# Performance work log

Measured on AMD Instinct MI355X. Metric: run time of the kernel, lower is better.

## Reference

```python
import jax, jax.numpy as jnp
import numpy as np


def hsigmoid(x):
    # ReLU6(x + 3) / 6
    return jnp.clip(x + 3.0, 0.0, 6.0) / 6.0


def setup_inputs() -> dict:
    key = jax.random.key(0)
    k1, k2 = jax.random.split(key)
    B, C, H, W = 16, 256, 128, 128
    K = 7
    x = jax.random.normal(k1, (B, C, H, W), dtype=jnp.float32)
    # Kaiming-ish small init for the 2->1 7x7 conv
    conv_w = jax.random.normal(k2, (1, 2, K, K), dtype=jnp.float32) * (1.0 / np.sqrt(2 * K * K))
    conv_b = jnp.zeros((1,), dtype=jnp.float32)
    return {"x": x, "conv_w": conv_w, "conv_b": conv_b}


def reference(x, conv_w, conv_b):
    # channel-wise max and mean -> [B, 1, H, W] each
    max_x = jnp.max(x, axis=1, keepdims=True)
    avg_x = jnp.mean(x, axis=1, keepdims=True)
    out = jnp.concatenate([max_x, avg_x], axis=1)  # [B, 2, H, W]
    # 7x7 conv, stride 1, padding = k//2 (SAME for odd k)
    pad = conv_w.shape[-1] // 2
    out = jax.lax.conv_general_dilated(
        out, conv_w,
        window_strides=(1, 1),
        padding=[(pad, pad), (pad, pad)],
        dimension_numbers=("NCHW", "OIHW", "NCHW"),
    ) + conv_b[None, :, None, None]  # [B, 1, H, W]
    gate = hsigmoid(out)
    return x * gate  # broadcast over channel dim
```

## Files before the change

### kernel.cpp

```cpp
#include <hip/hip_runtime.h>
#include <math.h>

#define HW      128
#define PLANE   16384
#define CHS     256
#define BATCH   16
#define CSTRIDE 16384
#define BSTRIDE (256 * 16384)
#define CHUNK_B 4

typedef float vf4 __attribute__((ext_vector_type(4)));

__global__ __launch_bounds__(256) void reduce_kernel(
    const float* __restrict__ x, float* __restrict__ pmax, float* __restrict__ pavg,
    int b0)
{
    const int tid = threadIdx.x;
    const int sc  = tid & 31;
    const int cg  = tid >> 5;
    const int g   = blockIdx.x * 32 + sc;
    const int b   = b0 + (g >> 12);
    const int sp  = (g & 4095) << 2;

    const float* xp = x + (size_t)b * BSTRIDE + sp + (size_t)(cg << 5) * CSTRIDE;

    float4 vmax = make_float4(-INFINITY, -INFINITY, -INFINITY, -INFINITY);
    float4 vsum = make_float4(0.f, 0.f, 0.f, 0.f);

    #pragma unroll 8
    for (int c = 0; c < 32; ++c) {
        const float4 v = *(const float4*)(xp + (size_t)c * CSTRIDE);
        vmax.x = fmaxf(vmax.x, v.x); vmax.y = fmaxf(vmax.y, v.y);
        vmax.z = fmaxf(vmax.z, v.z); vmax.w = fmaxf(vmax.w, v.w);
        vsum.x += v.x; vsum.y += v.y; vsum.z += v.z; vsum.w += v.w;
    }

    __shared__ float4 smax[256];
    __shared__ float4 ssum[256];
    smax[tid] = vmax;
    ssum[tid] = vsum;
    __syncthreads();

    if (tid < 32) {
        float4 m = smax[tid];
        float4 s = ssum[tid];
        #pragma unroll
        for (int j = 1; j < 8; ++j) {
            const float4 mj = smax[tid + 32 * j];
            const float4 sj = ssum[tid + 32 * j];
            m.x = fmaxf(m.x, mj.x); m.y = fmaxf(m.y, mj.y);
            m.z = fmaxf(m.z, mj.z); m.w = fmaxf(m.w, mj.w);
            s.x += sj.x; s.y += sj.y; s.z += sj.z; s.w += sj.w;
        }
        const float inv = 1.0f / 256.0f;
        s.x *= inv; s.y *= inv; s.z *= inv; s.w *= inv;
        const int gg = blockIdx.x * 32 + tid;
        const int bb = b0 + (gg >> 12);
        const int ss = (gg & 4095) << 2;
        *(float4*)(pmax + (size_t)bb * PLANE + ss) = m;
        *(float4*)(pavg + (size_t)bb * PLANE + ss) = s;
    }
}

__global__ __launch_bounds__(256) void gate_mul_kernel(
    const float* __restrict__ x,
    const float* __restrict__ pmax, const float* __restrict__ pavg,
    const float* __restrict__ cw, const float* __restrict__ cb,
    float* __restrict__ out, int b0)
{
    __shared__ float sw[98];
    __shared__ __align__(16) float sgate[HW];

    const int tid = threadIdx.x;
    if (tid < 98) sw[tid] = cw[tid];
    const int b = b0 + (blockIdx.x >> 7);
    const int h = blockIdx.x & 127;
    __syncthreads();

    if (tid < HW) {
        const int w = tid;
        float acc = cb[0];
        const float* pm = pmax + (size_t)b * PLANE;
        const float* pa = pavg + (size_t)b * PLANE;
        #pragma unroll
        for (int ky = 0; ky < 7; ++ky) {
            const int hh = h + ky - 3;
            if (hh >= 0 && hh < HW) {
                const float* prm = pm + hh * HW;
                const float* pra = pa + hh * HW;
                #pragma unroll
                for (int kx = 0; kx < 7; ++kx) {
                    const int ww = w + kx - 3;
                    if (ww >= 0 && ww < HW) {
                        acc = fmaf(sw[ky * 7 + kx],      prm[ww], acc);
                        acc = fmaf(sw[49 + ky * 7 + kx], pra[ww], acc);
                    }
                }
            }
        }
        sgate[w] = fminf(fmaxf(acc + 3.0f, 0.0f), 6.0f) * (1.0f / 6.0f);
    }
    __syncthreads();

    const int wc   = tid & 31;
    const int csub = tid >> 5;
    const float4 g4 = *(const float4*)(sgate + wc * 4);
    const size_t rowbase = (size_t)b * BSTRIDE + (size_t)h * HW + wc * 4;

    #pragma unroll 4
    for (int c = csub; c < CHS; c += 8) {
        const size_t off = rowbase + (size_t)c * CSTRIDE;
        const float4 v = *(const float4*)(x + off);
        vf4 r;
        r.x = v.x * g4.x; r.y = v.y * g4.y; r.z = v.z * g4.z; r.w = v.w * g4.w;
        __builtin_nontemporal_store(r, (vf4*)(out + off));
    }
}

extern "C" void kernel_launch(void* const* d_in, const int* in_sizes, int n_in,
                              void* d_out, int out_size, void* d_ws, size_t ws_size,
                              hipStream_t stream)
{
    const float* x  = (const float*)d_in[0];
    const float* cw = (const float*)d_in[1];
    const float* cb = (const float*)d_in[2];
    float* out = (float*)d_out;

    float* pmax = (float*)d_ws;
    float* pavg = pmax + (size_t)BATCH * PLANE;

    for (int b0 = 0; b0 < BATCH; b0 += CHUNK_B) {
        reduce_kernel<<<512, 256, 0, stream>>>(x, pmax, pavg, b0);
        gate_mul_kernel<<<CHUNK_B * 128, 256, 0, stream>>>(x, pmax, pavg, cw, cb, out, b0);
    }
}
```

Measured before the change: 499.2 us.

## Split conv-gate and channel multiply into separate kernels for wider parallelism

Separates the 7x7 conv + hsigmoid gate computation from the broadcast multiply, writing the gate plane to workspace. The multiply kernel now launches 1024 blocks over all channels and spatial positions, instead of 512 blocks in which half the threads sat idle during the conv. This aims to raise occupancy and memory-level parallelism on the bandwidth-bound multiply. The cost is an extra kernel launch per chunk and a small gate-plane round trip through memory.

```diff
diff --git a/kernel.cpp b/kernel.cpp
--- a/kernel.cpp
+++ b/kernel.cpp
@@ -62,54 +62,58 @@
     }
 }
 
-__global__ __launch_bounds__(256) void gate_mul_kernel(
-    const float* __restrict__ x,
+__global__ __launch_bounds__(128) void conv_gate_kernel(
     const float* __restrict__ pmax, const float* __restrict__ pavg,
     const float* __restrict__ cw, const float* __restrict__ cb,
-    float* __restrict__ out, int b0)
+    float* __restrict__ gate, int b0)
 {
     __shared__ float sw[98];
-    __shared__ __align__(16) float sgate[HW];
-
     const int tid = threadIdx.x;
     if (tid < 98) sw[tid] = cw[tid];
     const int b = b0 + (blockIdx.x >> 7);
     const int h = blockIdx.x & 127;
     __syncthreads();
 
-    if (tid < HW) {
-        const int w = tid;
-        float acc = cb[0];
-        const float* pm = pmax + (size_t)b * PLANE;
-        const float* pa = pavg + (size_t)b * PLANE;
-        #pragma unroll
-        for (int ky = 0; ky < 7; ++ky) {
-            const int hh = h + ky - 3;
-            if (hh >= 0 && hh < HW) {
-                const float* prm = pm + hh * HW;
-                const float* pra = pa + hh * HW;
-                #pragma unroll
-                for (int kx = 0; kx < 7; ++kx) {
-                    const int ww = w + kx - 3;
-                    if (ww >= 0 && ww < HW) {
-                        acc = fmaf(sw[ky * 7 + kx],      prm[ww], acc);
-                        acc = fmaf(sw[49 + ky * 7 + kx], pra[ww], acc);
-                    }
+    const int w = tid;
+    float acc = cb[0];
+    const float* pm = pmax + (size_t)b * PLANE;
+    const float* pa = pavg + (size_t)b * PLANE;
+    #pragma unroll
+    for (int ky = 0; ky < 7; ++ky) {
+        const int hh = h + ky - 3;
+        if (hh >= 0 && hh < HW) {
+            const float* prm = pm + hh * HW;
+            const float* pra = pa + hh * HW;
+            #pragma unroll
+            for (int kx = 0; kx < 7; ++kx) {
+                const int ww = w + kx - 3;
+                if (ww >= 0 && ww < HW) {
+                    acc = fmaf(sw[ky * 7 + kx],      prm[ww], acc);
+                    acc = fmaf(sw[49 + ky * 7 + kx], pra[ww], acc);
                 }
             }
         }
-        sgate[w] = fminf(fmaxf(acc + 3.0f, 0.0f), 6.0f) * (1.0f / 6.0f);
     }
-    __syncthreads();
+    gate[(size_t)b * PLANE + h * HW + w] =
+        fminf(fmaxf(acc + 3.0f, 0.0f), 6.0f) * (1.0f / 6.0f);
+}
 
-    const int wc   = tid & 31;
-    const int csub = tid >> 5;
-    const float4 g4 = *(const float4*)(sgate + wc * 4);
-    const size_t rowbase = (size_t)b * BSTRIDE + (size_t)h * HW + wc * 4;
+__global__ __launch_bounds__(256) void mul_kernel(
+    const float* __restrict__ x, const float* __restrict__ gate,
+    float* __restrict__ out, int b0)
+{
+    const int gt = blockIdx.x * 256 + threadIdx.x;
+    const int sc = gt & 16383;
+    const int cp = gt >> 14;
+    const int b  = b0 + (sc >> 12);
+    const int sp = (sc & 4095) << 2;
+
+    const float4 g4 = *(const float4*)(gate + (size_t)b * PLANE + sp);
+    const size_t base = (size_t)b * BSTRIDE + sp;
 
     #pragma unroll 4
-    for (int c = csub; c < CHS; c += 8) {
-        const size_t off = rowbase + (size_t)c * CSTRIDE;
+    for (int c = cp; c < CHS; c += 16) {
+        const size_t off = base + (size_t)c * CSTRIDE;
         const float4 v = *(const float4*)(x + off);
         vf4 r;
         r.x = v.x * g4.x; r.y = v.y * g4.y; r.z = v.z * g4.z; r.w = v.w * g4.w;
@@ -128,9 +132,11 @@
 
     float* pmax = (float*)d_ws;
     float* pavg = pmax + (size_t)BATCH * PLANE;
+    float* gate = pavg + (size_t)BATCH * PLANE;
 
     for (int b0 = 0; b0 < BATCH; b0 += CHUNK_B) {
         reduce_kernel<<<512, 256, 0, stream>>>(x, pmax, pavg, b0);
-        gate_mul_kernel<<<CHUNK_B * 128, 256, 0, stream>>>(x, pmax, pavg, cw, cb, out, b0);
+        conv_gate_kernel<<<CHUNK_B * 128, 128, 0, stream>>>(pmax, pavg, cw, cb, gate, b0);
+        mul_kernel<<<1024, 256, 0, stream>>>(x, gate, out, b0);
     }
 }
```

Result: slower. 510.8 us (+2.3%).
